# Kernel optimization log

Measured on AMD Instinct MI355X. Metric: run time of the kernel, lower is better.

## Reference

```python
import jax, jax.numpy as jnp
import numpy as np

RMS_EPS = 1e-6
GN_EPS = 1e-5


def rmsnorm(x, w):
    xf = x.astype(jnp.float32)
    y = xf * jax.lax.rsqrt(jnp.mean(xf * xf, axis=-1, keepdims=True) + RMS_EPS)
    return y.astype(x.dtype) * w


def multihead_layernorm(h, w):
    # h: [B,T,NH,DH]; GroupNorm with groups=NH -> LayerNorm over DH per head
    hf = h.astype(jnp.float32)
    mu = jnp.mean(hf, axis=-1, keepdims=True)
    var = jnp.var(hf, axis=-1, keepdims=True)
    y = (hf - mu) * jax.lax.rsqrt(var + GN_EPS)
    return (y * w).astype(h.dtype)


def slstm_layer(xn, W_gates, R_gates, b_gates, gn_w):
    # xn: [B,T,D]; W_gates/R_gates: [4,NH,DH,DH]; b_gates: [4,NH,DH]
    B, T, D = xn.shape
    _, NH, DH, _ = W_gates.shape
    xh = xn.reshape(B, T, NH, DH)
    # precompute input-driven gate preactivations: [T,B,4,NH,DH]
    gx = jnp.einsum('btnh,gnkh->tbgnk', xh, W_gates) + b_gates

    def step(carry, xt):
        c, n, h, m = carry
        rec = jnp.einsum('bnh,gnkh->bgnk', h, R_gates)  # [B,4,NH,DH]
        pre = xt + rec
        ipre, fpre, zpre, opre = pre[:, 0], pre[:, 1], pre[:, 2], pre[:, 3]
        m_new = jnp.maximum(fpre + m, ipre)  # log-space stabilizer
        igate = jnp.exp(ipre - m_new)
        fgate = jnp.exp(fpre + m - m_new)
        c_new = fgate * c + igate * jnp.tanh(zpre)
        n_new = fgate * n + igate
        h_new = jax.nn.sigmoid(opre) * c_new / n_new
        return (c_new, n_new, h_new, m_new), h_new

    zero = jnp.zeros((B, NH, DH), jnp.float32)
    carry0 = (zero, zero, zero, zero)
    _, hs = jax.lax.scan(step, carry0, gx)  # hs: [T,B,NH,DH]
    h = multihead_layernorm(hs.transpose(1, 0, 2, 3), gn_w)  # [B,T,NH,DH]
    return h.reshape(B, T, D)


def setup_inputs() -> dict:
    key = jax.random.key(0)
    B, T, D, NH = 8, 2048, 1024, 4
    DH = D // NH
    F = 2752
    ks = jax.random.split(key, 8)
    scale = 0.02
    return {
        'x': jax.random.normal(ks[0], (B, T, D), jnp.float32),
        'ln1_w': jnp.ones((D,), jnp.float32),
        'W_gates': jax.random.normal(ks[1], (4, NH, DH, DH), jnp.float32) * scale,
        'R_gates': jax.random.normal(ks[2], (4, NH, DH, DH), jnp.float32) * scale,
        'b_gates': jnp.zeros((4, NH, DH), jnp.float32),
        'gn_w': jnp.ones((NH, DH), jnp.float32),
        'ln2_w': jnp.ones((D,), jnp.float32),
        'Wg': jax.random.normal(ks[3], (D, F), jnp.float32) * scale,
        'Wu': jax.random.normal(ks[4], (D, F), jnp.float32) * scale,
        'Wd': jax.random.normal(ks[5], (F, D), jnp.float32) * scale,
    }


def reference(x, ln1_w, W_gates, R_gates, b_gates, gn_w, ln2_w, Wg, Wu, Wd):
    # x = x + sLSTM(RMSNorm(x))
    x = x + slstm_layer(rmsnorm(x, ln1_w), W_gates, R_gates, b_gates, gn_w)
    # x = x + SwiGLU_FFN(RMSNorm(x))
    y = rmsnorm(x, ln2_w)
    ff = (jax.nn.silu(y @ Wg) * (y @ Wu)) @ Wd
    return x + ff
```

## Files before the change

### kernel.cpp

```cpp
#include <hip/hip_runtime.h>
#include <hip/hip_bf16.h>

#define DEV __device__ __forceinline__

typedef __attribute__((ext_vector_type(4))) float f32x4;
typedef __attribute__((ext_vector_type(8))) short short8;
typedef __attribute__((ext_vector_type(8))) _Float16 f16x8;
typedef __attribute__((ext_vector_type(4))) int i32x4;
typedef __attribute__((ext_vector_type(4))) unsigned short u16x4;
typedef __attribute__((ext_vector_type(8))) unsigned short u16x8;

typedef __attribute__((address_space(3))) void lds_void;
typedef const __attribute__((address_space(1))) void g_void;
#define GLOAD16(g, l) __builtin_amdgcn_global_load_lds((g_void*)(g), (lds_void*)(l), 16, 0, 0)

DEV unsigned short f2h(float f){ union{_Float16 h; unsigned short u;} c; c.h = (_Float16)f; return c.u; }
DEV float h2f(unsigned short u){ union{unsigned short u; _Float16 h;} c; c.u = u; return (float)c.h; }
DEV f16x8 as_f16x8(short8 s){ union{short8 s; f16x8 h;} c; c.s = s; return c.h; }
DEV float fexp2(float x){
#if __has_builtin(__builtin_amdgcn_exp2f)
  return __builtin_amdgcn_exp2f(x);
#else
  return exp2f(x);
#endif
}
DEV float frcp(float x){
#if __has_builtin(__builtin_amdgcn_rcpf)
  return __builtin_amdgcn_rcpf(x);
#else
  return 1.f/x;
#endif
}
DEV float wsum(float v){
  #pragma unroll
  for(int o=32;o;o>>=1) v += __shfl_xor(v,o,64);
  return v;
}
DEV float wmax_(float v){
  #pragma unroll
  for(int o=32;o;o>>=1) v = fmaxf(v,__shfl_xor(v,o,64));
  return v;
}
DEV int swz(int row, int unit){ return row*64 + ((unit ^ ((row>>1)&3))<<4); }

__global__ __launch_bounds__(256) void prep_wbt(const float* __restrict__ W,
    const float* __restrict__ BG, unsigned short* __restrict__ WBT, float* __restrict__ BIAS){
  int bid = blockIdx.x;
  int g = bid>>10, n = (bid>>8)&3, k = bid&255;
  int C = (k<<2) | g;
  int h = threadIdx.x;
  WBT[((size_t)n*1024 + C)*256 + h] = f2h(W[(size_t)bid*256 + h]);
  if (h==0) BIAS[n*1024 + C] = BG[(g*4+n)*256 + k];
}

__global__ __launch_bounds__(256) void prep_rq(const float* __restrict__ R,
    signed char* __restrict__ RQ, float* __restrict__ SC){
  int bid = blockIdx.x;
  int g = bid>>10, n = (bid>>8)&3, k = bid&255;
  int h = threadIdx.x;
  float v = R[(size_t)bid*256 + h];
  float a = fabsf(v);
  float m = wmax_(a);
  __shared__ float red[4];
  int wv = threadIdx.x>>6, l = threadIdx.x&63;
  if (!l) red[wv] = m;
  __syncthreads();
  m = fmaxf(fmaxf(red[0],red[1]), fmaxf(red[2],red[3]));
  float s = fmaxf(m, 1e-20f) * (1.f/127.f);
  int q = (int)rintf(v/s);
  q = q > 127 ? 127 : (q < -127 ? -127 : q);
  int w  = k>>5, kblk = (k>>4)&1, f = (kblk<<2)|g, kf = h>>6;
  int ln = (k&15) | (((h>>4)&3)<<4);
  int j  = h&15;
  RQ[ (((size_t)(n*8+w)*32 + (f*4+kf))*64 + ln)*16 + j ] = (signed char)q;
  if (h==0) SC[n*1024 + g*256 + k] = s * (1.f/127.f);
}

__global__ __launch_bounds__(256) void transpose_cast(const float* __restrict__ IN,
    unsigned short* __restrict__ OUT, int K, int N){
  __shared__ float tile[32][33];
  int n0 = blockIdx.x*32, k0 = blockIdx.y*32;
  int c = threadIdx.x&31, r4 = threadIdx.x>>5;
  #pragma unroll
  for (int rr = r4; rr < 32; rr += 8) tile[rr][c] = IN[(size_t)(k0+rr)*N + n0 + c];
  __syncthreads();
  #pragma unroll
  for (int rr = r4; rr < 32; rr += 8) OUT[(size_t)(n0+rr)*K + k0 + c] = f2h(tile[c][rr]);
}

__global__ __launch_bounds__(256) void rmsnorm_k(const float* __restrict__ X,
    const float* __restrict__ W, unsigned short* __restrict__ O){
  size_t row = blockIdx.x;
  const f32x4* xp = (const f32x4*)(X + row*1024);
  f32x4 v = xp[threadIdx.x];
  float s = v[0]*v[0]+v[1]*v[1]+v[2]*v[2]+v[3]*v[3];
  s = wsum(s);
  __shared__ float red[4];
  int wv = threadIdx.x>>6, l = threadIdx.x&63;
  if (!l) red[wv] = s;
  __syncthreads();
  float tot = red[0]+red[1]+red[2]+red[3];
  float rs = rsqrtf(tot*(1.f/1024.f) + 1e-6f);
  int c = threadIdx.x*4;
  u16x4 o;
  #pragma unroll
  for (int j=0;j<4;j++) o[j] = f2h(v[j]*rs*W[c+j]);
  size_t orow = (row & 2047)*8 + (row >> 11);
  *(u16x4*)(O + orow*1024 + c) = o;
}

__global__ __launch_bounds__(256,2) void gemm0_k(
    const unsigned short* __restrict__ A, const unsigned short* __restrict__ B1,
    unsigned short* __restrict__ OB, const float* __restrict__ BIAS){
  __shared__ __align__(16) char smem[32768];
  char* smA = smem;
  char* smB = smem + 8192;
  int tid = threadIdx.x, w = tid>>6, l = tid&63;
  int n0 = blockIdx.x*128, m0 = blockIdx.y*128, head = blockIdx.z;
  A += (size_t)head*256; B1 += (size_t)head*1024*256;
  f32x4 acc[4][4];
  f32x4 z = {0.f,0.f,0.f,0.f};
  #pragma unroll
  for (int mi=0;mi<4;mi++)
    #pragma unroll
    for (int ni=0;ni<4;ni++) acc[mi][ni]=z;
  int wr = w>>1, wc = w&1;
  for (int kt = 0; kt < 256; kt += 32){
    #pragma unroll
    for (int c2=0;c2<2;c2++){
      int p = c2*256 + tid;
      int rr = p>>2, u = (p&3) ^ ((rr>>1)&3);
      int ldsb = (c2*256 + w*64)*16;
      GLOAD16(A  + (size_t)(m0+rr)*1024 + kt + u*8, smA + ldsb);
      GLOAD16(B1 + (size_t)(n0+rr)*256  + kt + u*8, smB + ldsb);
    }
    __syncthreads();
    short8 af[4], bf[4];
    #pragma unroll
    for (int mi=0;mi<4;mi++) af[mi] = *(const short8*)(smA + swz(wr*64 + mi*16 + (l&15), l>>4));
    #pragma unroll
    for (int ni=0;ni<4;ni++) bf[ni] = *(const short8*)(smB + swz(wc*64 + ni*16 + (l&15), l>>4));
    #pragma unroll
    for (int mi=0;mi<4;mi++)
      #pragma unroll
      for (int ni=0;ni<4;ni++)
        acc[mi][ni] = __builtin_amdgcn_mfma_f32_16x16x32_f16(as_f16x8(af[mi]), as_f16x8(bf[ni]), acc[mi][ni], 0,0,0);
    __syncthreads();
  }
  unsigned short* gt = (unsigned short*)smem;
  #pragma unroll
  for (int mi=0;mi<4;mi++)
    #pragma unroll
    for (int ni=0;ni<4;ni++)
      #pragma unroll
      for (int j=0;j<4;j++){
        int rr = wr*64 + mi*16 + (l>>4)*4 + j;
        int cc = wc*64 + ni*16 + (l&15);
        int Cp = n0 + cc;
        int g = Cp & 3, b = rr & 7;
        float fac = (g==2) ? 2.8853900817779268f : 1.4426950408889634f;
        gt[ (rr>>3)*1024 + (cc>>2)*32 + (b>>1)*8 + (b&1)*4 + g ]
          = f2h((acc[mi][ni][j] + BIAS[head*1024 + Cp]) * fac);
      }
  __syncthreads();
  int t0 = blockIdx.y*16, k0 = blockIdx.x*32;
  int t_loc = tid>>4, seg = tid&15;
  const u16x8* src = (const u16x8*)(gt + t_loc*1024 + seg*64);
  u16x8* dst = (u16x8*)(OB + ((((size_t)(t0+t_loc)*4 + head)*256 + k0)*32) + seg*64);
  #pragma unroll
  for (int i=0;i<8;i++) dst[i] = src[i];
}

#define SCAN_STEP(HR, HW, GXV, TT) do{                                          \
    i32x4 af[4];                                                                \
    _Pragma("unroll")                                                           \
    for (int kf=0;kf<4;kf++) af[kf] = *(const i32x4*)(&HR[ra + kf*64]);         \
    i32x4 acc[4];                                                               \
    _Pragma("unroll")                                                           \
    for (int g=0; g<4; g++){                                                    \
      i32x4 a = {0,0,0,0};                                                      \
      _Pragma("unroll")                                                         \
      for (int kf=0; kf<4; kf++)                                                \
        a = __builtin_amdgcn_mfma_i32_16x16x64_i8(af[kf], wf[g][kf], a, 0,0,0); \
      acc[g] = a;                                                               \
    }                                                                           \
    float ip2 = fmaf(sch[0],(float)acc[0][0], fmaf(scl[0],(float)acc[0][1], h2f(GXV[0]))); \
    float fpv = fmaf(sch[1],(float)acc[1][0], fmaf(scl[1],(float)acc[1][1], h2f(GXV[1]))) + ms; \
    float zp2 = fmaf(sch[2],(float)acc[2][0], fmaf(scl[2],(float)acc[2][1], h2f(GXV[2]))); \
    float op2 = fmaf(sch[3],(float)acc[3][0], fmaf(scl[3],(float)acc[3][1], h2f(GXV[3]))); \
    float mn = fmaxf(fpv, ip2);                                                 \
    float ig = fexp2(ip2 - mn);                                                 \
    float fg = fexp2(fpv - mn);                                                 \
    float e2 = fexp2(zp2);                                                      \
    float tz = fmaf(-2.f, frcp(e2 + 1.f), 1.f);                                 \
    float eo = fexp2(-op2);                                                     \
    float c  = fmaf(ig, tz, fg*cs);                                             \
    float nn = fmaf(fg, ns_, ig);                                               \
    float h  = c * frcp((1.f + eo)*nn);                                         \
    cs=c; ns_=nn; ms=mn;                                                        \
    float h127 = h*127.f;                                                       \
    float hiq = rintf(h127);                                                    \
    float loq = rintf((h127 - hiq)*127.f);                                      \
    HW[r_hi] = (signed char)(int)hiq;                                           \
    HW[r_lo] = (signed char)(int)loq;                                           \
    HS[(size_t)(TT)*8192 + hoff] = f2h(h);                                      \
  }while(0)

DEV void slow_spin(int* f, int n){
  while (__hip_atomic_load(f, __ATOMIC_RELAXED, __HIP_MEMORY_SCOPE_AGENT) < n)
    __builtin_amdgcn_s_sleep(127);
  (void)__hip_atomic_load(f, __ATOMIC_ACQUIRE, __HIP_MEMORY_SCOPE_AGENT);
}

DEV void sig_wait(int* f, int tid){
  asm volatile("s_waitcnt vmcnt(0) lgkmcnt(0)" ::: "memory");
  __syncthreads();
  if (tid==0){
    __hip_atomic_fetch_add(f, 1, __ATOMIC_RELEASE, __HIP_MEMORY_SCOPE_AGENT);
    slow_spin(f, 248);
  }
  __syncthreads();
}

__global__ __launch_bounds__(1024,4) void mega_k(
    const unsigned short* GX, const signed char* RQ, const float* SC,
    unsigned short* HS, int* FLAGS,
    const float* X, const float* GNW, const float* LN2W,
    const unsigned short* WGT, const unsigned short* WUT, const unsigned short* WDT,
    char* CHUNK0, float* X2OUT){
  __shared__ __align__(16) char smem[86016];
  int tid = threadIdx.x;
  const float L2E = 1.44269504f;

  if (blockIdx.x < 8){
    int bid = blockIdx.x;
    int n = bid >> 1, bg = bid & 1;
    int w = tid>>6, l = tid&63;
    signed char* hlA = (signed char*)smem;
    signed char* hlB = (signed char*)(smem + 4352);
    for (int i = tid; i < 8704; i += 1024) smem[i] = 0;

    int l15 = l & 15, q = l >> 4;
    i32x4 wf[4][4];
    {
      const i32x4* rp = (const i32x4*)RQ + (size_t)(n*8 + (w>>1))*32*64;
      #pragma unroll
      for (int g=0; g<4; g++){
        int f = ((w&1)<<2) | g;
        #pragma unroll
        for (int kf=0; kf<4; kf++)
          wf[g][kf] = rp[(f*4+kf)*64 + l];
      }
    }
    float sch[4], scl[4];
    {
      const float facs[4] = {1.4426950408889634f, 1.4426950408889634f,
                             2.8853900817779268f, 1.4426950408889634f};
      #pragma unroll
      for (int g=0; g<4; g++){
        float s = SC[n*1024 + g*256 + w*16 + l15] * facs[g];
        sch[g] = s; scl[g] = s*(1.f/127.f);
      }
    }
    float cs = 0.f, ns_ = 0.f, ms = 0.f;
    int goff = (n*256 + w*16 + l15)*32 + (bg*2 + (q>>1))*8 + (q&1)*4;
    int hoff = (n*8 + bg*4 + q)*256 + w*16 + l15;
    int ra   = l15*272 + q*16;
    int r_hi = (4*q + 0)*272 + w*16 + l15;
    int r_lo = r_hi + 272;

    u16x4 gxr = *(const u16x4*)(GX + goff);
    __syncthreads();

    for (int t = 0; t < 2048; t += 2){
      u16x4 gx1 = *(const u16x4*)(GX + (size_t)(t+1)*32768 + goff);
      SCAN_STEP(hlA, hlB, gxr, t);
      asm volatile("s_waitcnt lgkmcnt(0)" ::: "memory");
      __builtin_amdgcn_s_barrier();
      __builtin_amdgcn_sched_barrier(0);
      int tt2 = (t+2 < 2048) ? (t+2) : 2047;
      gxr = *(const u16x4*)(GX + (size_t)tt2*32768 + goff);
      SCAN_STEP(hlB, hlA, gx1, t+1);
      asm volatile("s_waitcnt lgkmcnt(0)" ::: "memory");
      __builtin_amdgcn_s_barrier();
      __builtin_amdgcn_sched_barrier(0);
      if (((t+2) & 255) == 0){
        asm volatile("s_waitcnt vmcnt(0)" ::: "memory");
        __builtin_amdgcn_s_barrier();
        if (tid == 0)
          __hip_atomic_fetch_add(&FLAGS[(t+1)>>8], 1, __ATOMIC_RELEASE, __HIP_MEMORY_SCOPE_AGENT);
      }
    }
  } else {
    int wid = blockIdx.x - 8;
    int w = tid>>6, l = tid&63;
    int wr = w>>2, wc = w&3;
    char* smA0 = smem;
    char* smB0 = smem + 16384;
    char* smC0 = smem + 20480;
    char* smA1 = smem + 24576;
    char* smB1b= smem + 40960;
    char* smC1 = smem + 45056;
    float* red = (float*)(smem + 49152);

    int pA = w*64 + l, rA = pA>>2, uA = (pA&3)^((rA>>1)&3);
    int w4 = w & 3;
    int pB = w4*64 + l, rB = pB>>2, uB = (pB&3)^((rB>>1)&3);

    for (int c = 0; c < 8; ++c){
      char* cb = CHUNK0 + (size_t)c*16777216;
      unsigned short* y2c = (unsigned short*)cb;
      unsigned short* Sc  = (unsigned short*)(cb + 4194304);

      if (tid==0) slow_spin(&FLAGS[c], 8);
      __syncthreads();

      {
        int hn = tid>>8, hk = tid&255;
        for (int r = wid; r < 2048; r += 248){
          int b = r>>8, tl = r&255, t = c*256 + tl;
          float v = h2f(HS[(((size_t)t*4+hn)*8+b)*256 + hk]);
          float s1 = wsum(v), s2 = wsum(v*v);
          if (!(tid&63)){ red[tid>>6] = s1; red[16+(tid>>6)] = s2; }
          __syncthreads();
          float sum = 0.f, sq = 0.f;
          #pragma unroll
          for (int i=0;i<4;i++){ sum += red[hn*4+i]; sq += red[16+hn*4+i]; }
          float mu = sum*(1.f/256.f);
          float var = sq*(1.f/256.f) - mu*mu;
          float rs = rsqrtf(var + 1e-5f);
          size_t xi = (size_t)(b*2048+t)*1024 + tid;
          float x2v = X[xi] + (v-mu)*rs*GNW[tid];
          X2OUT[xi] = x2v;
          float qq = wsum(x2v*x2v);
          if (!(tid&63)) red[32+(tid>>6)] = qq;
          __syncthreads();
          float tot = 0.f;
          #pragma unroll
          for (int i=0;i<16;i++) tot += red[32+i];
          float rs2 = rsqrtf(tot*(1.f/1024.f) + 1e-6f);
          y2c[(size_t)r*1024 + tid] = f2h(x2v*rs2*LN2W[tid]);
          __syncthreads();
        }
      }
      sig_wait(&FLAGS[8+c], tid);

      for (int task = wid; task < 344; task += 248){
        int mt = task/43, nt = task - mt*43;
        const unsigned short* A  = y2c + (size_t)mt*256*1024;
        const unsigned short* B1 = WGT + (size_t)nt*64*1024;
        const unsigned short* B2 = WUT + (size_t)nt*64*1024;
        f32x4 acc[4], acc2[4];
        f32x4 z = {0.f,0.f,0.f,0.f};
        #pragma unroll
        for (int mi=0;mi<4;mi++){ acc[mi]=z; acc2[mi]=z; }
        auto g1stage = [&](char* sa, char* sb, char* sc, int KT){
          GLOAD16(A + (size_t)rA*1024 + KT + uA*8, sa + w*1024);
          if (w < 4)      GLOAD16(B1 + (size_t)rB*1024 + KT + uB*8, sb + w4*1024);
          else if (w < 8) GLOAD16(B2 + (size_t)rB*1024 + KT + uB*8, sc + w4*1024);
        };
        auto g1comp = [&](char* sa, char* sb, char* sc){
          short8 af[4], bf, bg;
          #pragma unroll
          for (int mi=0;mi<4;mi++) af[mi] = *(const short8*)(sa + swz(wr*64 + mi*16 + (l&15), l>>4));
          bf = *(const short8*)(sb + swz(wc*16 + (l&15), l>>4));
          bg = *(const short8*)(sc + swz(wc*16 + (l&15), l>>4));
          #pragma unroll
          for (int mi=0;mi<4;mi++){
            acc[mi]  = __builtin_amdgcn_mfma_f32_16x16x32_f16(as_f16x8(af[mi]), as_f16x8(bf), acc[mi], 0,0,0);
            acc2[mi] = __builtin_amdgcn_mfma_f32_16x16x32_f16(as_f16x8(af[mi]), as_f16x8(bg), acc2[mi], 0,0,0);
          }
        };
        g1stage(smA0, smB0, smC0, 0);
        __syncthreads();
        for (int kt = 0; kt < 1024; kt += 64){
          g1stage(smA1, smB1b, smC1, kt+32);
          g1comp(smA0, smB0, smC0);
          __syncthreads();
          if (kt+64 < 1024) g1stage(smA0, smB0, smC0, kt+64);
          g1comp(smA1, smB1b, smC1);
          __syncthreads();
        }
        #pragma unroll
        for (int mi=0;mi<4;mi++)
          #pragma unroll
          for (int j=0;j<4;j++){
            int gr = wr*64 + mi*16 + (l>>4)*4 + j;
            int gc = nt*64 + wc*16 + (l&15);
            float v = acc[mi][j], u2 = acc2[mi][j];
            float sg = v*frcp(1.f + fexp2(-v*L2E));
            Sc[(size_t)(mt*256+gr)*2752 + gc] = f2h(sg*u2);
          }
      }
      sig_wait(&FLAGS[16+c], tid);

      for (int task = wid; task < 128; task += 248){
        int mt = task>>4, nt = task&15;
        const unsigned short* A = Sc  + (size_t)mt*256*2752;
        const unsigned short* B = WDT + (size_t)nt*64*2752;
        f32x4 acc[4];
        f32x4 z = {0.f,0.f,0.f,0.f};
        #pragma unroll
        for (int mi=0;mi<4;mi++) acc[mi]=z;
        auto g2stage = [&](char* sa, char* sb, int KT){
          GLOAD16(A + (size_t)rA*2752 + KT + uA*8, sa + w*1024);
          if (w < 4) GLOAD16(B + (size_t)rB*2752 + KT + uB*8, sb + w4*1024);
        };
        auto g2comp = [&](char* sa, char* sb){
          short8 af[4], bf;
          #pragma unroll
          for (int mi=0;mi<4;mi++) af[mi] = *(const short8*)(sa + swz(wr*64 + mi*16 + (l&15), l>>4));
          bf = *(const short8*)(sb + swz(wc*16 + (l&15), l>>4));
          #pragma unroll
          for (int mi=0;mi<4;mi++)
            acc[mi] = __builtin_amdgcn_mfma_f32_16x16x32_f16(as_f16x8(af[mi]), as_f16x8(bf), acc[mi], 0,0,0);
        };
        g2stage(smA0, smB0, 0);
        __syncthreads();
        for (int kt = 0; kt < 2752; kt += 64){
          g2stage(smA1, smB1b, kt+32);
          g2comp(smA0, smB0);
          __syncthreads();
          if (kt+64 < 2752) g2stage(smA0, smB0, kt+64);
          g2comp(smA1, smB1b);
          __syncthreads();
        }
        #pragma unroll
        for (int mi=0;mi<4;mi++)
          #pragma unroll
          for (int j=0;j<4;j++){
            int gr = wr*64 + mi*16 + (l>>4)*4 + j;
            int gc = nt*64 + wc*16 + (l&15);
            size_t idx = (size_t)(mt*2048 + c*256 + gr)*1024 + gc;
            X2OUT[idx] = X2OUT[idx] + acc[mi][j];
          }
      }
    }
  }
}

extern "C" void kernel_launch(void* const* d_in, const int* in_sizes, int n_in,
                              void* d_out, int out_size, void* d_ws, size_t ws_size,
                              hipStream_t stream){
  (void)in_sizes; (void)n_in; (void)out_size;
  const float* x    = (const float*)d_in[0];
  const float* ln1w = (const float*)d_in[1];
  const float* Wg_  = (const float*)d_in[2];
  const float* Rg_  = (const float*)d_in[3];
  const float* bg_  = (const float*)d_in[4];
  const float* gnw  = (const float*)d_in[5];
  const float* ln2w = (const float*)d_in[6];
  const float* Wgf  = (const float*)d_in[7];
  const float* Wuf  = (const float*)d_in[8];
  const float* Wdf  = (const float*)d_in[9];
  float* out = (float*)d_out;
  char* ws = (char*)d_ws;

  if (ws_size < 187858944ull) return;
  unsigned short* wbt = (unsigned short*)(ws + 0);
  float*          bias= (float*)        (ws + 2097152);
  int*            flags=(int*)          (ws + 2097152);
  signed char*    rq  = (signed char*)  (ws + 2113536);
  float*          sc2 = (float*)        (ws + 3162112);
  unsigned short* wgt = (unsigned short*)(ws + 3178496);
  unsigned short* wut = (unsigned short*)(ws + 8814592);
  unsigned short* wdt = (unsigned short*)(ws + 14450688);
  unsigned short* xn  = (unsigned short*)(ws + 20086784);
  unsigned short* hs  = (unsigned short*)(ws + 20086784);
  unsigned short* gx  = (unsigned short*)(ws + 53641216);

  prep_wbt<<<4096,256,0,stream>>>(Wg_, bg_, wbt, bias);
  prep_rq <<<4096,256,0,stream>>>(Rg_, rq, sc2);
  transpose_cast<<<dim3(86,32),256,0,stream>>>(Wgf, wgt, 1024, 2752);
  transpose_cast<<<dim3(86,32),256,0,stream>>>(Wuf, wut, 1024, 2752);
  transpose_cast<<<dim3(32,86),256,0,stream>>>(Wdf, wdt, 2752, 1024);

  rmsnorm_k<<<16384,256,0,stream>>>(x, ln1w, xn);
  gemm0_k<<<dim3(8,128,4),256,0,stream>>>(xn, wbt, gx, bias);
  hipMemsetAsync(flags, 0, 128, stream);
  mega_k<<<256,1024,0,stream>>>(gx, rq, sc2, hs, flags, x, gnw, ln2w,
                                wgt, wut, wdt, (char*)gx, out);
}
```

Before: 1.946 ms.

## Split final scan chunks into halves to shorten FFN tail after recurrence

The scan-to-FFN pipeline now uses 9 chunks instead of 8: the last 256 timesteps are split into two 128-step chunks, so the scan signals earlier and less FFN work remains after the recurrence finishes. Chunk offsets, row mappings and flag indices are generalized to match, and the flag memset is enlarged. GEMM loop barriers also change from __syncthreads to an explicit vmcnt wait plus s_barrier. The risk is extra sync overhead, and the 128-step chunks give only 4 GEMM1 M-tiles (172 tasks) over 248 worker blocks, so utilization is lower in that tail.

After: 1.961 ms. Within noise of the previous version (+0.8%).

```diff
diff --git a/kernel.cpp b/kernel.cpp
--- a/kernel.cpp
+++ b/kernel.cpp
@@ -13,6 +13,8 @@
 typedef __attribute__((address_space(3))) void lds_void;
 typedef const __attribute__((address_space(1))) void g_void;
 #define GLOAD16(g, l) __builtin_amdgcn_global_load_lds((g_void*)(g), (lds_void*)(l), 16, 0, 0)
+#define PHASE_BAR() do{ asm volatile("s_waitcnt vmcnt(0)" ::: "memory"); \
+  __builtin_amdgcn_s_barrier(); __builtin_amdgcn_sched_barrier(0); }while(0)
 
 DEV unsigned short f2h(float f){ union{_Float16 h; unsigned short u;} c; c.h = (_Float16)f; return c.u; }
 DEV float h2f(unsigned short u){ union{unsigned short u; _Float16 h;} c; c.u = u; return (float)c.h; }
@@ -284,11 +286,17 @@
       asm volatile("s_waitcnt lgkmcnt(0)" ::: "memory");
       __builtin_amdgcn_s_barrier();
       __builtin_amdgcn_sched_barrier(0);
-      if (((t+2) & 255) == 0){
-        asm volatile("s_waitcnt vmcnt(0)" ::: "memory");
-        __builtin_amdgcn_s_barrier();
-        if (tid == 0)
-          __hip_atomic_fetch_add(&FLAGS[(t+1)>>8], 1, __ATOMIC_RELEASE, __HIP_MEMORY_SCOPE_AGENT);
+      {
+        int tp = t + 2;
+        int pc = -1;
+        if (tp <= 1792){ if ((tp & 255) == 0) pc = (tp>>8) - 1; }
+        else if ((tp & 127) == 0) pc = 7 + ((tp - 1920)>>7);
+        if (pc >= 0){
+          asm volatile("s_waitcnt vmcnt(0)" ::: "memory");
+          __builtin_amdgcn_s_barrier();
+          if (tid == 0)
+            __hip_atomic_fetch_add(&FLAGS[pc], 1, __ATOMIC_RELEASE, __HIP_MEMORY_SCOPE_AGENT);
+        }
       }
     }
   } else {
@@ -307,18 +315,24 @@
     int w4 = w & 3;
     int pB = w4*64 + l, rB = pB>>2, uB = (pB&3)^((rB>>1)&3);
 
-    for (int c = 0; c < 8; ++c){
-      char* cb = CHUNK0 + (size_t)c*16777216;
+    const int t0s[9]  = {0,256,512,768,1024,1280,1536,1792,1920};
+    const int lens[9] = {256,256,256,256,256,256,256,128,128};
+
+    for (int c = 0; c < 9; ++c){
+      int t0 = t0s[c], len = lens[c];
+      int lenlog = (len == 256) ? 8 : 7;
+      int rows = len*8;
+      char* cb = CHUNK0 + (size_t)t0*65536;
       unsigned short* y2c = (unsigned short*)cb;
-      unsigned short* Sc  = (unsigned short*)(cb + 4194304);
+      unsigned short* Sc  = (unsigned short*)(cb + (size_t)rows*2048);
 
       if (tid==0) slow_spin(&FLAGS[c], 8);
       __syncthreads();
 
       {
         int hn = tid>>8, hk = tid&255;
-        for (int r = wid; r < 2048; r += 248){
-          int b = r>>8, tl = r&255, t = c*256 + tl;
+        for (int r = wid; r < rows; r += 248){
+          int b = r>>lenlog, tl = r&(len-1), t = t0 + tl;
           float v = h2f(HS[(((size_t)t*4+hn)*8+b)*256 + hk]);
           float s1 = wsum(v), s2 = wsum(v*v);
           if (!(tid&63)){ red[tid>>6] = s1; red[16+(tid>>6)] = s2; }
@@ -343,9 +357,10 @@
           __syncthreads();
         }
       }
-      sig_wait(&FLAGS[8+c], tid);
-
-      for (int task = wid; task < 344; task += 248){
+      sig_wait(&FLAGS[16+c], tid);
+
+      int g1t = (rows>>8)*43;
+      for (int task = wid; task < g1t; task += 248){
         int mt = task/43, nt = task - mt*43;
         const unsigned short* A  = y2c + (size_t)mt*256*1024;
         const unsigned short* B1 = WGT + (size_t)nt*64*1024;
@@ -372,14 +387,14 @@
           }
         };
         g1stage(smA0, smB0, smC0, 0);
-        __syncthreads();
+        PHASE_BAR();
         for (int kt = 0; kt < 1024; kt += 64){
           g1stage(smA1, smB1b, smC1, kt+32);
           g1comp(smA0, smB0, smC0);
-          __syncthreads();
+          PHASE_BAR();
           if (kt+64 < 1024) g1stage(smA0, smB0, smC0, kt+64);
           g1comp(smA1, smB1b, smC1);
-          __syncthreads();
+          PHASE_BAR();
         }
         #pragma unroll
         for (int mi=0;mi<4;mi++)
@@ -392,9 +407,10 @@
             Sc[(size_t)(mt*256+gr)*2752 + gc] = f2h(sg*u2);
           }
       }
-      sig_wait(&FLAGS[16+c], tid);
-
-      for (int task = wid; task < 128; task += 248){
+      sig_wait(&FLAGS[32+c], tid);
+
+      int g2t = (rows>>8)*16;
+      for (int task = wid; task < g2t; task += 248){
         int mt = task>>4, nt = task&15;
         const unsigned short* A = Sc  + (size_t)mt*256*2752;
         const unsigned short* B = WDT + (size_t)nt*64*2752;
@@ -416,14 +432,14 @@
             acc[mi] = __builtin_amdgcn_mfma_f32_16x16x32_f16(as_f16x8(af[mi]), as_f16x8(bf), acc[mi], 0,0,0);
         };
         g2stage(smA0, smB0, 0);
-        __syncthreads();
+        PHASE_BAR();
         for (int kt = 0; kt < 2752; kt += 64){
           g2stage(smA1, smB1b, kt+32);
           g2comp(smA0, smB0);
-          __syncthreads();
+          PHASE_BAR();
           if (kt+64 < 2752) g2stage(smA0, smB0, kt+64);
           g2comp(smA1, smB1b);
-          __syncthreads();
+          PHASE_BAR();
         }
         #pragma unroll
         for (int mi=0;mi<4;mi++)
@@ -431,7 +447,9 @@
           for (int j=0;j<4;j++){
             int gr = wr*64 + mi*16 + (l>>4)*4 + j;
             int gc = nt*64 + wc*16 + (l&15);
-            size_t idx = (size_t)(mt*2048 + c*256 + gr)*1024 + gc;
+            int r = mt*256 + gr;
+            int b = r>>lenlog, tl = r&(len-1);
+            size_t idx = ((size_t)(b*2048 + t0 + tl))*1024 + gc;
             X2OUT[idx] = X2OUT[idx] + acc[mi][j];
           }
       }
@@ -477,7 +495,7 @@
 
   rmsnorm_k<<<16384,256,0,stream>>>(x, ln1w, xn);
   gemm0_k<<<dim3(8,128,4),256,0,stream>>>(xn, wbt, gx, bias);
-  hipMemsetAsync(flags, 0, 128, stream);
+  hipMemsetAsync(flags, 0, 256, stream);
   mega_k<<<256,1024,0,stream>>>(gx, rq, sc2, hs, flags, x, gnw, ln2w,
                                 wgt, wut, wdt, (char*)gx, out);
 }
```
